# Kernel tuning notes

Measured on AMD Instinct MI355X. Metric: run time of the kernel, lower is better.

## Reference

```python
import jax, jax.numpy as jnp
import numpy as np

DIM = 256
NUM_HEADS = 8
WINDOW = 7


def setup_inputs() -> dict:
    key = jax.random.key(0)
    ks = jax.random.split(key, 6)
    B, N, C = 4, 2048, DIM
    x = jax.random.normal(ks[0], (B, N, C), dtype=jnp.float32)
    qkv_w = jax.random.normal(ks[1], (3 * C, C), dtype=jnp.float32) * 0.02
    qkv_b = jax.random.normal(ks[2], (3 * C,), dtype=jnp.float32) * 0.02
    proj_w = jax.random.normal(ks[3], (C, C), dtype=jnp.float32) * 0.02
    proj_b = jax.random.normal(ks[4], (C,), dtype=jnp.float32) * 0.02
    bias_table = jax.random.normal(ks[5], ((2 * WINDOW - 1) * NUM_HEADS,), dtype=jnp.float32) * 0.02
    return {"x": x, "qkv_w": qkv_w, "qkv_b": qkv_b, "proj_w": proj_w,
            "proj_b": proj_b, "bias_table": bias_table}


def _rel_bias(bias_table, seq_len):
    w = WINDOW
    coords = jnp.arange(w)
    idx = coords[:, None] - coords[None, :] + (w - 1)  # (w, w), values in [0, 2w-2]
    # Faithful to original: table[idx.view(-1)].view(w,w,-1) -> last dim 1,
    # i.e. bias is shared across heads.
    bias = bias_table[idx]  # (w, w)
    if seq_len <= w:
        return bias[:seq_len, :seq_len]
    repeats = (seq_len + w - 1) // w
    bias = jnp.tile(bias, (repeats, repeats))[:seq_len, :seq_len]
    return bias  # (N, N)


def reference(x, qkv_w, qkv_b, proj_w, proj_b, bias_table):
    B, N, C = x.shape
    H, hd = NUM_HEADS, C // NUM_HEADS
    qkv = x @ qkv_w.T + qkv_b                       # (B, N, 3C)
    qkv = qkv.reshape(B, N, 3, H, hd).transpose(2, 0, 3, 1, 4)
    q, k, v = qkv[0], qkv[1], qkv[2]                # each (B, H, N, hd)
    scale = hd ** -0.5
    attn = jnp.einsum('bhnd,bhmd->bhnm', q, k) * scale  # (B, H, N, N)
    bias = _rel_bias(bias_table, N)                 # (N, N), shared across heads
    attn = attn + bias[None, None, :, :]
    attn = jax.nn.softmax(attn, axis=-1)
    out = jnp.einsum('bhnm,bhmd->bhnd', attn, v)    # (B, H, N, hd)
    out = out.transpose(0, 2, 1, 3).reshape(B, N, C)
    return out @ proj_w.T + proj_b
```

## Files before the change

### kernel.cpp

```cpp
#include <hip/hip_runtime.h>
#include <stdint.h>

#define DIMC   256
#define NHEADS 8
#define HD     32
#define BATCH  4
#define SEQ    2048
#define MTOT   (BATCH * SEQ)
#define QKVN   (MTOT * HD * NHEADS)
#define SCALE  0.17677669529663687f
#define LOG2E  1.4426950408889634f
#define SCL2E  (SCALE * LOG2E)

typedef short bf16x8 __attribute__((ext_vector_type(8)));
typedef float f32x4  __attribute__((ext_vector_type(4)));

#if defined(__has_builtin)
#if __has_builtin(__builtin_amdgcn_exp2f)
#define EXP2F __builtin_amdgcn_exp2f
#else
#define EXP2F exp2f
#endif
#else
#define EXP2F exp2f
#endif

static __device__ __forceinline__ unsigned short f2bf(float f) {
    unsigned int u = __float_as_uint(f);
    u += 0x7fffu + ((u >> 16) & 1u);
    return (unsigned short)(u >> 16);
}

static __device__ __forceinline__ unsigned int cvt2(float a, float b) {
#if defined(__has_builtin) && __has_builtin(__builtin_amdgcn_cvt_pk_bf16_f32)
    typedef __bf16 bf2 __attribute__((ext_vector_type(2)));
    bf2 v = __builtin_amdgcn_cvt_pk_bf16_f32(a, b);
    return __builtin_bit_cast(unsigned int, v);
#else
    return (unsigned int)f2bf(a) | ((unsigned int)f2bf(b) << 16);
#endif
}

#define NX8   262144
#define NWQ8  24576
#define NWP8  8192
#define NQA8  8192
#define NKA8  8192
#define NPREP (NX8 + NWQ8 + NWP8 + NQA8 + NKA8)

__global__ __launch_bounds__(256) void prep_kernel(
    const float* __restrict__ x, const float* __restrict__ wq,
    const float* __restrict__ wp, const float* __restrict__ table,
    unsigned short* __restrict__ xbf, unsigned short* __restrict__ wqbf,
    unsigned short* __restrict__ wpbf,
    unsigned short* __restrict__ QA, unsigned short* __restrict__ KA)
{
    int g = blockIdx.x * 256 + threadIdx.x;
    const float* src = nullptr;
    unsigned short* dst = nullptr;
    if (g < NX8)                      { src = x  + (size_t)g * 8;            dst = xbf  + (size_t)g * 8; }
    else if (g < NX8 + NWQ8)          { int l = g - NX8;        src = wq + (size_t)l * 8; dst = wqbf + (size_t)l * 8; }
    else if (g < NX8 + NWQ8 + NWP8)   { int l = g - NX8 - NWQ8; src = wp + (size_t)l * 8; dst = wpbf + (size_t)l * 8; }
    if (src) {
        float4 a0 = *(const float4*)src;
        float4 a1 = *(const float4*)(src + 4);
        uint4 pk;
        pk.x = cvt2(a0.x, a0.y); pk.y = cvt2(a0.z, a0.w);
        pk.z = cvt2(a1.x, a1.y); pk.w = cvt2(a1.z, a1.w);
        *(uint4*)dst = pk;
        return;
    }
    int l = g - (NX8 + NWQ8 + NWP8);
    if (l < NQA8) {
        int row = l >> 2, i0 = (l & 3) << 3, r7 = row % 7;
        unsigned short v[8];
        #pragma unroll
        for (int i = 0; i < 8; i++) v[i] = (i0 + i == r7) ? (unsigned short)0x3F80 : (unsigned short)0;
        *(uint4*)(QA + (size_t)row * 32 + i0) = *(const uint4*)v;
    } else if (l < NQA8 + NKA8) {
        l -= NQA8;
        int row = l >> 2, i0 = (l & 3) << 3, r7 = row % 7;
        unsigned short v[8];
        #pragma unroll
        for (int i = 0; i < 8; i++) {
            int ii = i0 + i;
            v[i] = (ii < 7) ? f2bf(table[ii - r7 + 6] * LOG2E) : (unsigned short)0;
        }
        *(uint4*)(KA + (size_t)row * 32 + i0) = *(const uint4*)v;
    }
}

__global__ __launch_bounds__(256) void gemm_qkv_kernel(
    const unsigned short* __restrict__ A,
    const unsigned short* __restrict__ W,
    const float* __restrict__ bias,
    unsigned short* __restrict__ qb,
    unsigned short* __restrict__ kb,
    unsigned short* __restrict__ vtb)
{
    __shared__ __align__(16) unsigned short FW[8][64][32];

    const int t    = threadIdx.x;
    const int wave = t >> 6;
    const int lane = t & 63;
    const int cg   = lane & 15;
    const int quad = lane >> 4;
    const int m0   = blockIdx.y * 128;
    const int n0   = blockIdx.x * 64;

    {
        int r  = t >> 2, cb = t & 3;
        int pc = (cb ^ ((r >> 1) & 3)) << 3;
        #pragma unroll
        for (int chunk = 0; chunk < 8; chunk++)
            *(bf16x8*)&FW[chunk][r][pc] =
                *(const bf16x8*)(W + (size_t)(n0 + r) * 256 + chunk * 32 + cb * 8);
    }
    __syncthreads();

    const unsigned short* Arow = A + (size_t)(m0 + wave * 16 + cg) * 256 + quad * 8;
    const int rsw = ((cg >> 1) & 3);

    f32x4 acc[2][4];
    #pragma unroll
    for (int s = 0; s < 2; s++)
        #pragma unroll
        for (int c = 0; c < 4; c++) acc[s][c] = (f32x4){0.f, 0.f, 0.f, 0.f};

    #pragma unroll
    for (int chunk = 0; chunk < 8; chunk++) {
        bf16x8 wf[4];
        #pragma unroll
        for (int c = 0; c < 4; c++)
            wf[c] = *(const bf16x8*)&FW[chunk][c * 16 + cg][(quad ^ rsw) << 3];
        #pragma unroll
        for (int s = 0; s < 2; s++) {
            bf16x8 af = *(const bf16x8*)(Arow + (size_t)s * 64 * 256 + chunk * 32);
            #pragma unroll
            for (int c = 0; c < 4; c++)
                acc[s][c] = __builtin_amdgcn_mfma_f32_16x16x32_bf16(af, wf[c], acc[s][c], 0, 0, 0);
        }
    }

    if (blockIdx.x >= 8) {
        float (*TR)[68] = (float (*)[68])(void*)&FW[0][0][0];
        #pragma unroll
        for (int s = 0; s < 2; s++) {
            __syncthreads();
            #pragma unroll
            for (int c = 0; c < 4; c++) {
                int l = c * 16 + cg;
                float bv = bias[n0 + l];
                float4 vv;
                vv.x = acc[s][c][0] + bv; vv.y = acc[s][c][1] + bv;
                vv.z = acc[s][c][2] + bv; vv.w = acc[s][c][3] + bv;
                *(float4*)__builtin_assume_aligned(&TR[l][wave * 16 + quad * 4], 16) = vv;
            }
            __syncthreads();
            int l  = t >> 2;
            int mm = (t & 3) << 4;
            int n  = n0 + l;
            int h  = (n >> 5) & 7;
            int d  = n & 31;
            int b_ = m0 >> 11;
            int nn = (m0 & 2047) + s * 64 + mm;
            const float* tr = (const float*)__builtin_assume_aligned(&TR[l][mm], 16);
            float4 v0 = *(const float4*)(tr);
            float4 v1 = *(const float4*)(tr + 4);
            float4 v2 = *(const float4*)(tr + 8);
            float4 v3 = *(const float4*)(tr + 12);
            uint4 pk0, pk1;
            pk0.x = cvt2(v0.x, v0.y); pk0.y = cvt2(v0.z, v0.w);
            pk0.z = cvt2(v1.x, v1.y); pk0.w = cvt2(v1.z, v1.w);
            pk1.x = cvt2(v2.x, v2.y); pk1.y = cvt2(v2.z, v2.w);
            pk1.z = cvt2(v3.x, v3.y); pk1.w = cvt2(v3.z, v3.w);
            unsigned short* dst = vtb + ((size_t)((b_ * NHEADS + h) * HD + d)) * SEQ + nn;
            *(uint4*)dst       = pk0;
            *(uint4*)(dst + 8) = pk1;
        }
        return;
    }

    #pragma unroll
    for (int s = 0; s < 2; s++) {
        #pragma unroll
        for (int c = 0; c < 4; c++) {
            int n = n0 + c * 16 + cg;
            float bv = bias[n];
            int which = n >> 8;
            int h     = (n >> 5) & 7;
            int d     = n & 31;
            #pragma unroll
            for (int rr = 0; rr < 4; rr++) {
                int m = m0 + s * 64 + wave * 16 + quad * 4 + rr;
                float val = acc[s][c][rr] + bv;
                int b_ = m >> 11;
                int nn = m & 2047;
                int bh = b_ * NHEADS + h;
                if (which == 0)
                    qb[((size_t)bh * SEQ + nn) * HD + d] = f2bf(val * SCL2E);
                else
                    kb[((size_t)bh * SEQ + nn) * HD + d] = f2bf(val);
            }
        }
    }
}

__global__ __launch_bounds__(256) void gemm_proj_kernel(
    const unsigned short* __restrict__ A,
    const unsigned short* __restrict__ W,
    const float* __restrict__ bias,
    float* __restrict__ outf)
{
    __shared__ __align__(16) unsigned short FW[8][64][32];

    const int t    = threadIdx.x;
    const int wave = t >> 6;
    const int lane = t & 63;
    const int cg   = lane & 15;
    const int quad = lane >> 4;
    const int m0   = blockIdx.y * 64;
    const int n0   = blockIdx.x * 64;

    {
        int r  = t >> 2, cb = t & 3;
        int pc = (cb ^ ((r >> 1) & 3)) << 3;
        #pragma unroll
        for (int chunk = 0; chunk < 8; chunk++)
            *(bf16x8*)&FW[chunk][r][pc] =
                *(const bf16x8*)(W + (size_t)(n0 + r) * 256 + chunk * 32 + cb * 8);
    }
    __syncthreads();

    const unsigned short* Arow = A + (size_t)(m0 + wave * 16 + cg) * 256 + quad * 8;
    const int rsw = ((cg >> 1) & 3);

    f32x4 acc[4];
    #pragma unroll
    for (int c = 0; c < 4; c++) acc[c] = (f32x4){0.f, 0.f, 0.f, 0.f};

    #pragma unroll
    for (int chunk = 0; chunk < 8; chunk++) {
        bf16x8 af = *(const bf16x8*)(Arow + chunk * 32);
        bf16x8 wf[4];
        #pragma unroll
        for (int c = 0; c < 4; c++)
            wf[c] = *(const bf16x8*)&FW[chunk][c * 16 + cg][(quad ^ rsw) << 3];
        #pragma unroll
        for (int c = 0; c < 4; c++)
            acc[c] = __builtin_amdgcn_mfma_f32_16x16x32_bf16(af, wf[c], acc[c], 0, 0, 0);
    }

    #pragma unroll
    for (int c = 0; c < 4; c++) {
        int n = n0 + c * 16 + cg;
        float bv = bias[n];
        #pragma unroll
        for (int rr = 0; rr < 4; rr++) {
            int m = m0 + wave * 16 + quad * 4 + rr;
            outf[(size_t)m * 256 + n] = acc[c][rr] + bv;
        }
    }
}

__global__ __launch_bounds__(256) void attn_mfma_kernel(
    const unsigned short* __restrict__ Q,
    const unsigned short* __restrict__ K,
    const unsigned short* __restrict__ Vt,
    const unsigned short* __restrict__ QA,
    const unsigned short* __restrict__ KA,
    unsigned short* __restrict__ AO)
{
    __shared__ __align__(16) unsigned short PL[4][64][72];

    const int t    = threadIdx.x;
    const int wave = t >> 6;
    const int lane = t & 63;
    const int cg   = lane & 15;
    const int quad = lane >> 4;

    const int bid = blockIdx.x;
    const int qt  = bid & 31;
    const int bh  = bid >> 5;
    const int b   = bh >> 3;
    const int h   = bh & 7;
    const int q0  = qt * 64;

    const unsigned short* Kbase = K  + (size_t)bh * (SEQ * HD);
    const unsigned short* Vbase = Vt + (size_t)bh * (SEQ * HD);

    bf16x8 qf[4], qfa[4];
    #pragma unroll
    for (int qi = 0; qi < 4; qi++) {
        qf[qi]  = *(const bf16x8*)(Q + (size_t)bh * (SEQ * HD) +
                                   (size_t)(q0 + qi * 16 + cg) * HD + quad * 8);
        qfa[qi] = *(const bf16x8*)(QA + (size_t)(q0 + qi * 16 + cg) * HD + quad * 8);
    }

    bf16x8 ones;
    #pragma unroll
    for (int i = 0; i < 8; i++) ones[i] = (short)0x3F80;

    f32x4 o[4][2], ol[4];
    #pragma unroll
    for (int qi = 0; qi < 4; qi++) {
        o[qi][0] = (f32x4){0.f, 0.f, 0.f, 0.f};
        o[qi][1] = (f32x4){0.f, 0.f, 0.f, 0.f};
        ol[qi]   = (f32x4){0.f, 0.f, 0.f, 0.f};
    }

    const int kstart = wave * (SEQ / 4);
    #pragma unroll 2
    for (int jj = 0; jj < SEQ / 4; jj += 64) {
        const int j0 = kstart + jj;

        bf16x8 kf[4], kfa[4];
        #pragma unroll
        for (int jt = 0; jt < 4; jt++) {
            kf[jt]  = *(const bf16x8*)(Kbase + (size_t)(j0 + jt * 16 + cg) * HD + quad * 8);
            kfa[jt] = *(const bf16x8*)(KA    + (size_t)(j0 + jt * 16 + cg) * HD + quad * 8);
        }
        bf16x8 vf[2][2];
        #pragma unroll
        for (int kt = 0; kt < 2; kt++)
            #pragma unroll
            for (int dt = 0; dt < 2; dt++)
                vf[kt][dt] = *(const bf16x8*)(Vbase + (size_t)(dt * 16 + cg) * SEQ +
                                              j0 + kt * 32 + quad * 8);

        #pragma unroll
        for (int half = 0; half < 2; half++) {
            f32x4 s[2][4];
            #pragma unroll
            for (int qh = 0; qh < 2; qh++) {
                int qi = half * 2 + qh;
                #pragma unroll
                for (int jt = 0; jt < 4; jt++) {
                    s[qh][jt] = __builtin_amdgcn_mfma_f32_16x16x32_bf16(
                        kfa[jt], qfa[qi], (f32x4){0.f, 0.f, 0.f, 0.f}, 0, 0, 0);
                    s[qh][jt] = __builtin_amdgcn_mfma_f32_16x16x32_bf16(
                        kf[jt], qf[qi], s[qh][jt], 0, 0, 0);
                }
            }
            #pragma unroll
            for (int qh = 0; qh < 2; qh++) {
                int qi = half * 2 + qh;
                #pragma unroll
                for (int jt = 0; jt < 4; jt++) {
                    float p0 = EXP2F(s[qh][jt][0]);
                    float p1 = EXP2F(s[qh][jt][1]);
                    float p2 = EXP2F(s[qh][jt][2]);
                    float p3 = EXP2F(s[qh][jt][3]);
                    uint2 w;
                    w.x = cvt2(p0, p1);
                    w.y = cvt2(p2, p3);
                    *(uint2*)&PL[wave][qi * 16 + cg][jt * 16 + quad * 4] = w;
                }
            }
        }
        __builtin_amdgcn_s_waitcnt(0xC07F);

        #pragma unroll
        for (int qi = 0; qi < 4; qi++) {
            bf16x8 pa0 = *(const bf16x8*)&PL[wave][qi * 16 + cg][quad * 8];
            bf16x8 pa1 = *(const bf16x8*)&PL[wave][qi * 16 + cg][32 + quad * 8];
            o[qi][0] = __builtin_amdgcn_mfma_f32_16x16x32_bf16(pa0, vf[0][0], o[qi][0], 0, 0, 0);
            o[qi][0] = __builtin_amdgcn_mfma_f32_16x16x32_bf16(pa1, vf[1][0], o[qi][0], 0, 0, 0);
            o[qi][1] = __builtin_amdgcn_mfma_f32_16x16x32_bf16(pa0, vf[0][1], o[qi][1], 0, 0, 0);
            o[qi][1] = __builtin_amdgcn_mfma_f32_16x16x32_bf16(pa1, vf[1][1], o[qi][1], 0, 0, 0);
            ol[qi]   = __builtin_amdgcn_mfma_f32_16x16x32_bf16(pa0, ones, ol[qi], 0, 0, 0);
            ol[qi]   = __builtin_amdgcn_mfma_f32_16x16x32_bf16(pa1, ones, ol[qi], 0, 0, 0);
        }
    }

    __builtin_amdgcn_s_waitcnt(0xC07F);
    float* OPw = (float*)&PL[wave][0][0];
    #pragma unroll
    for (int qi = 0; qi < 4; qi++) {
        #pragma unroll
        for (int dt = 0; dt < 2; dt++)
            #pragma unroll
            for (int rr = 0; rr < 4; rr++)
                OPw[(qi * 16 + quad * 4 + rr) * 33 + dt * 16 + cg] = o[qi][dt][rr];
        if (cg == 0) {
            #pragma unroll
            for (int rr = 0; rr < 4; rr++)
                OPw[(qi * 16 + quad * 4 + rr) * 33 + 32] = ol[qi][rr];
        }
    }
    __syncthreads();

    {
        int q  = t >> 2;
        int d0 = (t & 3) << 3;
        float l = 0.f;
        float ov[8];
        #pragma unroll
        for (int i = 0; i < 8; i++) ov[i] = 0.f;
        #pragma unroll
        for (int w = 0; w < 4; w++) {
            const float* OPx = (const float*)&PL[w][0][0];
            l += OPx[q * 33 + 32];
            #pragma unroll
            for (int i = 0; i < 8; i++) ov[i] += OPx[q * 33 + d0 + i];
        }
        float inv = 1.f / l;
        unsigned short pk[8];
        #pragma unroll
        for (int i = 0; i < 8; i += 2) {
            unsigned int u = cvt2(ov[i] * inv, ov[i + 1] * inv);
            pk[i]     = (unsigned short)(u & 0xffffu);
            pk[i + 1] = (unsigned short)(u >> 16);
        }
        *(uint4*)(AO + ((size_t)(b * SEQ + q0 + q)) * DIMC + h * HD + d0) = *(const uint4*)pk;
    }
}

extern "C" void kernel_launch(void* const* d_in, const int* in_sizes, int n_in,
                              void* d_out, int out_size, void* d_ws, size_t ws_size,
                              hipStream_t stream) {
    const float* x      = (const float*)d_in[0];
    const float* qkv_w  = (const float*)d_in[1];
    const float* qkv_b  = (const float*)d_in[2];
    const float* proj_w = (const float*)d_in[3];
    const float* proj_b = (const float*)d_in[4];
    const float* table  = (const float*)d_in[5];
    float* out = (float*)d_out;

    unsigned short* ws   = (unsigned short*)d_ws;
    unsigned short* qb   = ws;
    unsigned short* kb   = qb  + (size_t)QKVN;
    unsigned short* vtb  = kb  + (size_t)QKVN;
    unsigned short* ao   = vtb + (size_t)QKVN;
    unsigned short* xbf  = ao  + (size_t)QKVN;
    unsigned short* wqbf = xbf + (size_t)QKVN;
    unsigned short* wpbf = wqbf + 196608;
    unsigned short* QAt  = wpbf + 65536;
    unsigned short* KAt  = QAt  + 65536;

    prep_kernel<<<dim3((NPREP + 255) / 256), 256, 0, stream>>>(
        x, qkv_w, proj_w, table, xbf, wqbf, wpbf, QAt, KAt);

    gemm_qkv_kernel<<<dim3(768 / 64, MTOT / 128), 256, 0, stream>>>(
        xbf, wqbf, qkv_b, qb, kb, vtb);

    attn_mfma_kernel<<<dim3(BATCH * NHEADS * (SEQ / 64)), 256, 0, stream>>>(
        qb, kb, vtb, QAt, KAt, ao);

    gemm_proj_kernel<<<dim3(256 / 64, MTOT / 64), 256, 0, stream>>>(
        ao, wpbf, proj_b, out);
}
```

Measured before the change: 130.4 us.

## Fuse fp32-to-bf16 conversion into GEMMs and build bias operands in-kernel

Drops the separate prep kernel. The QKV and projection GEMMs now load fp32 inputs and weights and convert them to bf16 on the fly. The attention kernel builds the relative-bias one-hot Q augmentation in registers and stages a 7-row K-augment table in shared memory, indexed by position mod 7. This removes one launch and the round-trip of bf16 copies through global memory. In exchange, the QKV GEMM reads x as fp32 (twice the bytes) and converts it per tile, and each x tile is re-read and re-converted by all 12 column blocks.

Result: no change. 130.9 us (+0.3%).

```diff
diff --git a/kernel.cpp b/kernel.cpp
--- a/kernel.cpp
+++ b/kernel.cpp
@@ -41,58 +41,18 @@
 #endif
 }
 
-#define NX8   262144
-#define NWQ8  24576
-#define NWP8  8192
-#define NQA8  8192
-#define NKA8  8192
-#define NPREP (NX8 + NWQ8 + NWP8 + NQA8 + NKA8)
-
-__global__ __launch_bounds__(256) void prep_kernel(
-    const float* __restrict__ x, const float* __restrict__ wq,
-    const float* __restrict__ wp, const float* __restrict__ table,
-    unsigned short* __restrict__ xbf, unsigned short* __restrict__ wqbf,
-    unsigned short* __restrict__ wpbf,
-    unsigned short* __restrict__ QA, unsigned short* __restrict__ KA)
-{
-    int g = blockIdx.x * 256 + threadIdx.x;
-    const float* src = nullptr;
-    unsigned short* dst = nullptr;
-    if (g < NX8)                      { src = x  + (size_t)g * 8;            dst = xbf  + (size_t)g * 8; }
-    else if (g < NX8 + NWQ8)          { int l = g - NX8;        src = wq + (size_t)l * 8; dst = wqbf + (size_t)l * 8; }
-    else if (g < NX8 + NWQ8 + NWP8)   { int l = g - NX8 - NWQ8; src = wp + (size_t)l * 8; dst = wpbf + (size_t)l * 8; }
-    if (src) {
-        float4 a0 = *(const float4*)src;
-        float4 a1 = *(const float4*)(src + 4);
-        uint4 pk;
-        pk.x = cvt2(a0.x, a0.y); pk.y = cvt2(a0.z, a0.w);
-        pk.z = cvt2(a1.x, a1.y); pk.w = cvt2(a1.z, a1.w);
-        *(uint4*)dst = pk;
-        return;
-    }
-    int l = g - (NX8 + NWQ8 + NWP8);
-    if (l < NQA8) {
-        int row = l >> 2, i0 = (l & 3) << 3, r7 = row % 7;
-        unsigned short v[8];
-        #pragma unroll
-        for (int i = 0; i < 8; i++) v[i] = (i0 + i == r7) ? (unsigned short)0x3F80 : (unsigned short)0;
-        *(uint4*)(QA + (size_t)row * 32 + i0) = *(const uint4*)v;
-    } else if (l < NQA8 + NKA8) {
-        l -= NQA8;
-        int row = l >> 2, i0 = (l & 3) << 3, r7 = row % 7;
-        unsigned short v[8];
-        #pragma unroll
-        for (int i = 0; i < 8; i++) {
-            int ii = i0 + i;
-            v[i] = (ii < 7) ? f2bf(table[ii - r7 + 6] * LOG2E) : (unsigned short)0;
-        }
-        *(uint4*)(KA + (size_t)row * 32 + i0) = *(const uint4*)v;
-    }
+static __device__ __forceinline__ bf16x8 ld8f_bf(const float* p) {
+    float4 a0 = *(const float4*)p;
+    float4 a1 = *(const float4*)(p + 4);
+    uint4 pk;
+    pk.x = cvt2(a0.x, a0.y); pk.y = cvt2(a0.z, a0.w);
+    pk.z = cvt2(a1.x, a1.y); pk.w = cvt2(a1.z, a1.w);
+    return __builtin_bit_cast(bf16x8, pk);
 }
 
 __global__ __launch_bounds__(256) void gemm_qkv_kernel(
-    const unsigned short* __restrict__ A,
-    const unsigned short* __restrict__ W,
+    const float* __restrict__ A,
+    const float* __restrict__ W,
     const float* __restrict__ bias,
     unsigned short* __restrict__ qb,
     unsigned short* __restrict__ kb,
@@ -114,11 +74,11 @@
         #pragma unroll
         for (int chunk = 0; chunk < 8; chunk++)
             *(bf16x8*)&FW[chunk][r][pc] =
-                *(const bf16x8*)(W + (size_t)(n0 + r) * 256 + chunk * 32 + cb * 8);
+                ld8f_bf(W + (size_t)(n0 + r) * 256 + chunk * 32 + cb * 8);
     }
     __syncthreads();
 
-    const unsigned short* Arow = A + (size_t)(m0 + wave * 16 + cg) * 256 + quad * 8;
+    const float* Arow = A + (size_t)(m0 + wave * 16 + cg) * 256 + quad * 8;
     const int rsw = ((cg >> 1) & 3);
 
     f32x4 acc[2][4];
@@ -135,7 +95,7 @@
             wf[c] = *(const bf16x8*)&FW[chunk][c * 16 + cg][(quad ^ rsw) << 3];
         #pragma unroll
         for (int s = 0; s < 2; s++) {
-            bf16x8 af = *(const bf16x8*)(Arow + (size_t)s * 64 * 256 + chunk * 32);
+            bf16x8 af = ld8f_bf(Arow + (size_t)s * 64 * 256 + chunk * 32);
             #pragma unroll
             for (int c = 0; c < 4; c++)
                 acc[s][c] = __builtin_amdgcn_mfma_f32_16x16x32_bf16(af, wf[c], acc[s][c], 0, 0, 0);
@@ -208,7 +168,7 @@
 
 __global__ __launch_bounds__(256) void gemm_proj_kernel(
     const unsigned short* __restrict__ A,
-    const unsigned short* __restrict__ W,
+    const float* __restrict__ W,
     const float* __restrict__ bias,
     float* __restrict__ outf)
 {
@@ -228,7 +188,7 @@
         #pragma unroll
         for (int chunk = 0; chunk < 8; chunk++)
             *(bf16x8*)&FW[chunk][r][pc] =
-                *(const bf16x8*)(W + (size_t)(n0 + r) * 256 + chunk * 32 + cb * 8);
+                ld8f_bf(W + (size_t)(n0 + r) * 256 + chunk * 32 + cb * 8);
     }
     __syncthreads();
 
@@ -267,11 +227,11 @@
     const unsigned short* __restrict__ Q,
     const unsigned short* __restrict__ K,
     const unsigned short* __restrict__ Vt,
-    const unsigned short* __restrict__ QA,
-    const unsigned short* __restrict__ KA,
+    const float* __restrict__ table,
     unsigned short* __restrict__ AO)
 {
     __shared__ __align__(16) unsigned short PL[4][64][72];
+    __shared__ __align__(16) unsigned short KA7[7][32];
 
     const int t    = threadIdx.x;
     const int wave = t >> 6;
@@ -286,6 +246,13 @@
     const int h   = bh & 7;
     const int q0  = qt * 64;
 
+    if (t < 224) {
+        int r = t >> 5, c = t & 31;
+        float v = (c < 7) ? table[c - r + 6] * LOG2E : 0.f;
+        KA7[r][c] = f2bf(v);
+    }
+    __syncthreads();
+
     const unsigned short* Kbase = K  + (size_t)bh * (SEQ * HD);
     const unsigned short* Vbase = Vt + (size_t)bh * (SEQ * HD);
 
@@ -294,7 +261,10 @@
     for (int qi = 0; qi < 4; qi++) {
         qf[qi]  = *(const bf16x8*)(Q + (size_t)bh * (SEQ * HD) +
                                    (size_t)(q0 + qi * 16 + cg) * HD + quad * 8);
-        qfa[qi] = *(const bf16x8*)(QA + (size_t)(q0 + qi * 16 + cg) * HD + quad * 8);
+        int p = (q0 + qi * 16 + cg) % 7;
+        #pragma unroll
+        for (int i = 0; i < 8; i++)
+            qfa[qi][i] = (quad == 0 && i == p) ? (short)0x3F80 : (short)0;
     }
 
     bf16x8 ones;
@@ -310,6 +280,10 @@
     }
 
     const int kstart = wave * (SEQ / 4);
+    int kb7[4];
+    #pragma unroll
+    for (int jt = 0; jt < 4; jt++) kb7[jt] = (kstart + jt * 16 + cg) % 7;
+
     #pragma unroll 2
     for (int jj = 0; jj < SEQ / 4; jj += 64) {
         const int j0 = kstart + jj;
@@ -318,7 +292,7 @@
         #pragma unroll
         for (int jt = 0; jt < 4; jt++) {
             kf[jt]  = *(const bf16x8*)(Kbase + (size_t)(j0 + jt * 16 + cg) * HD + quad * 8);
-            kfa[jt] = *(const bf16x8*)(KA    + (size_t)(j0 + jt * 16 + cg) * HD + quad * 8);
+            kfa[jt] = *(const bf16x8*)&KA7[kb7[jt]][quad * 8];
         }
         bf16x8 vf[2][2];
         #pragma unroll
@@ -371,6 +345,10 @@
             ol[qi]   = __builtin_amdgcn_mfma_f32_16x16x32_bf16(pa0, ones, ol[qi], 0, 0, 0);
             ol[qi]   = __builtin_amdgcn_mfma_f32_16x16x32_bf16(pa1, ones, ol[qi], 0, 0, 0);
         }
+
+        #pragma unroll
+        for (int jt = 0; jt < 4; jt++)
+            kb7[jt] = (kb7[jt] == 6) ? 0 : kb7[jt] + 1;
     }
 
     __builtin_amdgcn_s_waitcnt(0xC07F);
@@ -432,21 +410,13 @@
     unsigned short* kb   = qb  + (size_t)QKVN;
     unsigned short* vtb  = kb  + (size_t)QKVN;
     unsigned short* ao   = vtb + (size_t)QKVN;
-    unsigned short* xbf  = ao  + (size_t)QKVN;
-    unsigned short* wqbf = xbf + (size_t)QKVN;
-    unsigned short* wpbf = wqbf + 196608;
-    unsigned short* QAt  = wpbf + 65536;
-    unsigned short* KAt  = QAt  + 65536;
-
-    prep_kernel<<<dim3((NPREP + 255) / 256), 256, 0, stream>>>(
-        x, qkv_w, proj_w, table, xbf, wqbf, wpbf, QAt, KAt);
 
     gemm_qkv_kernel<<<dim3(768 / 64, MTOT / 128), 256, 0, stream>>>(
-        xbf, wqbf, qkv_b, qb, kb, vtb);
+        x, qkv_w, qkv_b, qb, kb, vtb);
 
     attn_mfma_kernel<<<dim3(BATCH * NHEADS * (SEQ / 64)), 256, 0, stream>>>(
-        qb, kb, vtb, QAt, KAt, ao);
+        qb, kb, vtb, table, ao);
 
     gemm_proj_kernel<<<dim3(256 / 64, MTOT / 64), 256, 0, stream>>>(
-        ao, wpbf, proj_b, out);
-}
+        ao, proj_w, proj_b, out);
+}
```
